# Optimization experiments

Hardware: AMD Instinct MI355X
Metric: run time of the kernel (lower is better)

The kernel has to match this reference:

```python
import jax, jax.numpy as jnp
import numpy as np

KS = 64      # kernel_size
NFFT = 64    # n_fft
IC = 32      # in_channel
OC = 64      # out_channel
B, T1, T2 = 4, 4096, 512


def setup_inputs() -> dict:
    key = jax.random.key(0)
    k1, k2, k3, k4 = jax.random.split(key, 4)
    x = jax.random.normal(k1, (B, T1, IC), dtype=jnp.float32)
    # continuous index in [0, T1-1)
    index = jax.random.uniform(k2, (B, T2), dtype=jnp.float32) * (T1 - 1)
    kb = 1.0 / np.sqrt(KS * IC)  # matches reset_parameters uniform bound
    kernel = jax.random.uniform(k3, (OC, IC, NFFT), minval=-kb, maxval=kb, dtype=jnp.float32)
    bias = jax.random.uniform(k4, (OC,), minval=-kb, maxval=kb, dtype=jnp.float32)
    return {"x": x, "index": index, "kernel": kernel, "bias": bias}


def reference(x, index, kernel, bias):
    # fractional-delay kernel per (b, t2) via FFT phase shift
    i = jnp.floor(index).astype(jnp.int32)          # (b, t2) integer part
    f = index - jnp.floor(index)                    # (b, t2) fractional part
    freqs = jnp.arange(NFFT // 2 + 1)               # rfft bins
    shift = jnp.exp(2j * jnp.pi * f[..., None] * freqs / NFFT)   # (b, t2, nf)
    K = jnp.fft.rfft(kernel)                        # (oc, ic, nf)
    K = K[None, None] * shift[:, :, None, None, :]  # (b, t2, oc, ic, nf)
    ker = jnp.fft.irfft(K, n=KS)                    # (b, t2, oc, ic, ks)

    # gather centered length-ks windows of x at integer positions i
    pad = KS // 2
    x_pad = jnp.pad(x, ((0, 0), (pad, pad), (0, 0)))            # (b, t1+2p, ic)
    pos = i[:, :, None] + jnp.arange(KS)[None, None, :]          # (b, t2, ks)
    barr = jnp.arange(x.shape[0])[:, None, None]
    xwin = x_pad[barr, pos]                                      # (b, t2, ks, ic)

    # per-position matmul: out[b,t,o] = sum_{c,k} ker[b,t,o,c,k] * xwin[b,t,k,c]
    out = jnp.einsum('btock,btkc->bto', ker, xwin) + bias
    return out
```

## Files before the change

### kernel.cpp

```cpp
#include <hip/hip_runtime.h>
#include <hip/hip_bf16.h>
#include <math.h>

#define B_   4
#define T1_  4096
#define T2_  512
#define IC_  32
#define OC_  64
#define KS_  64

typedef unsigned short u16;
typedef unsigned int   u32;
typedef __attribute__((ext_vector_type(8))) short  short8;
typedef __attribute__((ext_vector_type(4))) float  float4v;

__device__ __forceinline__ u16 f2bf(float f) {
    union { u32 u; float f; } v; v.f = f;
    u32 u = v.u;
    return (u16)((u + 0x7FFFu + ((u >> 16) & 1u)) >> 16);
}

#define PI_F 3.14159265358979323846f

__global__ __launch_bounds__(256) void prep_interp_kernel(
        const float* __restrict__ x, const float* __restrict__ index,
        const float* __restrict__ kern, u16* __restrict__ Y,
        u16* __restrict__ Bsz)
{
    __shared__ __align__(16) float w2[4][76];

    const int tid = threadIdx.x;

    if (blockIdx.x < 64) {
        int gid = blockIdx.x * 256 + tid;
        int o   = gid & 63;
        int cs8 = gid >> 6;
        const float* p = kern + (size_t)o * 2048 + cs8 * 8;
        float4 a = *(const float4*)p;
        float4 b = *(const float4*)(p + 4);
        u16* q = Bsz + (size_t)cs8 * 512 + o * 8;
        *(ushort4*)(q)     = make_ushort4(f2bf(a.x), f2bf(a.y), f2bf(a.z), f2bf(a.w));
        *(ushort4*)(q + 4) = make_ushort4(f2bf(b.x), f2bf(b.y), f2bf(b.z), f2bf(b.w));
        return;
    }

    const int pb   = blockIdx.x - 64;
    const int wv   = tid >> 6;
    const int lane = tid & 63;
    const int bt   = pb * 4 + wv;
    const int b    = bt >> 9;

    const float fidx = index[bt];
    const float flo  = floorf(fidx);
    const int   i0   = (int)flo;
    const float f    = fidx - flo;

    {
        const int t = lane;
        float wj;
        if (f <= 0.0f) {
            wj = (t == 0) ? 1.0f : 0.0f;
        } else {
            float spf = sinf(PI_F * f);
            float a   = PI_F * ((float)t + f) * (1.0f / 64.0f);
            wj = ((t & 1) ? -spf : spf) * cosf(a) / (64.0f * sinf(a));
        }
        w2[wv][t] = wj;
        if (t < 8) w2[wv][64 + t] = wj;
    }

    const int nm = lane & 15;
    const int q  = lane >> 4;

    short8 Afr[4];
    #pragma unroll
    for (int d = 0; d < 4; ++d) {
        const int o0 = (16 * d + q * 8 - nm) & 63;
        const float* wp = &w2[wv][o0];
        union { u16 u[8]; short8 s; } cv;
        #pragma unroll
        for (int j = 0; j < 8; ++j) cv.u[j] = f2bf(wp[j]);
        Afr[d] = cv.s;
    }

    short8 Bfr[2][2];
    #pragma unroll
    for (int kb = 0; kb < 2; ++kb) {
        #pragma unroll
        for (int nt = 0; nt < 2; ++nt) {
            const int c = nt * 16 + nm;
            union { u16 u[8]; short8 s; } cv;
            #pragma unroll
            for (int j = 0; j < 8; ++j) {
                int pos = i0 - 32 + kb * 32 + q * 8 + j;
                int pc  = min(max(pos, 0), T1_ - 1);
                float v = x[(size_t)(b * T1_ + pc) * IC_ + c];
                v = ((unsigned)pos < (unsigned)T1_) ? v : 0.0f;
                cv.u[j] = f2bf(v);
            }
            Bfr[kb][nt] = cv.s;
        }
    }

    float4v acc[4][2];
    #pragma unroll
    for (int mt = 0; mt < 4; ++mt)
        #pragma unroll
        for (int nt = 0; nt < 2; ++nt)
            acc[mt][nt] = (float4v){0.f, 0.f, 0.f, 0.f};
    #pragma unroll
    for (int kb = 0; kb < 2; ++kb)
        #pragma unroll
        for (int mt = 0; mt < 4; ++mt) {
            const int d = (2 * kb - mt) & 3;
            #pragma unroll
            for (int nt = 0; nt < 2; ++nt)
                acc[mt][nt] = __builtin_amdgcn_mfma_f32_16x16x32_bf16(
                                  Afr[d], Bfr[kb][nt], acc[mt][nt], 0, 0, 0);
        }

    #pragma unroll
    for (int mt = 0; mt < 4; ++mt)
        #pragma unroll
        for (int nt = 0; nt < 2; ++nt) {
            const int c = nt * 16 + nm;
            const int s = mt * 16 + q * 4;
            u32 d0 = (u32)f2bf(acc[mt][nt][0]) | ((u32)f2bf(acc[mt][nt][1]) << 16);
            u32 d1 = (u32)f2bf(acc[mt][nt][2]) | ((u32)f2bf(acc[mt][nt][3]) << 16);
            *(uint2*)(Y + (size_t)bt * 2048 + c * 64 + s) = make_uint2(d0, d1);
        }
}

__global__ __launch_bounds__(512, 2) void gemm_kernel(const u16* __restrict__ Y,
                                                      const u16* __restrict__ Bsz,
                                                      const float* __restrict__ bias,
                                                      float* __restrict__ out)
{
    __shared__ float red[8][4][16][17];

    const int tid  = threadIdx.x;
    const int w    = tid >> 6;
    const int lane = tid & 63;
    const int nm   = lane & 15;
    const int q    = lane >> 4;
    const int g    = blockIdx.x;

    const int pbA = (g & 7) + 8 * (4 * (g >> 3) + (nm >> 2));
    const int btA = 4 * pbA + (nm & 3);

    const int kb0 = w * 8;
    const u16* aptr = Y   + (size_t)btA * 2048 + kb0 * 32 + q * 8;
    const u16* bptr = Bsz + (size_t)kb0 * 2048 + q * 512 + nm * 8;

    short8 a[8], b[8][4];
    #pragma unroll
    for (int i = 0; i < 8; ++i) {
        a[i] = *(const short8*)(aptr + i * 32);
        #pragma unroll
        for (int n = 0; n < 4; ++n)
            b[i][n] = *(const short8*)(bptr + (size_t)i * 2048 + n * 128);
    }

    float4v acc0 = {0,0,0,0}, acc1 = {0,0,0,0}, acc2 = {0,0,0,0}, acc3 = {0,0,0,0};
    #pragma unroll
    for (int i = 0; i < 8; ++i) {
        acc0 = __builtin_amdgcn_mfma_f32_16x16x32_bf16(a[i], b[i][0], acc0, 0, 0, 0);
        acc1 = __builtin_amdgcn_mfma_f32_16x16x32_bf16(a[i], b[i][1], acc1, 0, 0, 0);
        acc2 = __builtin_amdgcn_mfma_f32_16x16x32_bf16(a[i], b[i][2], acc2, 0, 0, 0);
        acc3 = __builtin_amdgcn_mfma_f32_16x16x32_bf16(a[i], b[i][3], acc3, 0, 0, 0);
    }

    #pragma unroll
    for (int r = 0; r < 4; ++r) {
        const int row = q * 4 + r;
        red[w][0][row][nm] = acc0[r];
        red[w][1][row][nm] = acc1[r];
        red[w][2][row][nm] = acc2[r];
        red[w][3][row][nm] = acc3[r];
    }
    __syncthreads();

    #pragma unroll
    for (int e = tid; e < 1024; e += 512) {
        const int row = e >> 6;
        const int o   = e & 63;
        float s = bias[o];
        #pragma unroll
        for (int ww = 0; ww < 8; ++ww)
            s += red[ww][o >> 4][row][o & 15];
        const int pbo = (g & 7) + 8 * (4 * (g >> 3) + (row >> 2));
        const int bto = 4 * pbo + (row & 3);
        out[(size_t)bto * 64 + o] = s;
    }
}

extern "C" void kernel_launch(void* const* d_in, const int* in_sizes, int n_in,
                              void* d_out, int out_size, void* d_ws, size_t ws_size,
                              hipStream_t stream)
{
    const float* x     = (const float*)d_in[0];
    const float* index = (const float*)d_in[1];
    const float* kern  = (const float*)d_in[2];
    const float* bias  = (const float*)d_in[3];
    float* out = (float*)d_out;

    u16* Y   = (u16*)d_ws;
    u16* Bsz = (u16*)((char*)d_ws + (size_t)8 * 1024 * 1024);

    prep_interp_kernel<<<dim3(64 + B_ * T2_ / 4), dim3(256), 0, stream>>>(x, index, kern, Y, Bsz);
    gemm_kernel<<<dim3(128), dim3(512), 0, stream>>>(Y, Bsz, bias, out);
}
```

Baseline: 71.79 us.

## Fuse interpolation and kernel GEMM into one kernel with LDS-staged intermediate

After: 76.05 us. +5.9%, slower.

```diff
diff --git a/kernel.cpp b/kernel.cpp
--- a/kernel.cpp
+++ b/kernel.cpp
@@ -14,40 +14,29 @@
 typedef __attribute__((ext_vector_type(8))) short  short8;
 typedef __attribute__((ext_vector_type(4))) float  float4v;
 
+#define PI_F 3.14159265358979323846f
+
 __device__ __forceinline__ u16 f2bf(float f) {
     union { u32 u; float f; } v; v.f = f;
     u32 u = v.u;
     return (u16)((u + 0x7FFFu + ((u >> 16) & 1u)) >> 16);
 }
 
-#define PI_F 3.14159265358979323846f
-
-__global__ __launch_bounds__(256) void prep_interp_kernel(
+__global__ __launch_bounds__(512, 2) void fused_kernel(
         const float* __restrict__ x, const float* __restrict__ index,
-        const float* __restrict__ kern, u16* __restrict__ Y,
-        u16* __restrict__ Bsz)
+        const float* __restrict__ kern, const float* __restrict__ bias,
+        float* __restrict__ out)
 {
-    __shared__ __align__(16) float w2[4][76];
-
-    const int tid = threadIdx.x;
-
-    if (blockIdx.x < 64) {
-        int gid = blockIdx.x * 256 + tid;
-        int o   = gid & 63;
-        int cs8 = gid >> 6;
-        const float* p = kern + (size_t)o * 2048 + cs8 * 8;
-        float4 a = *(const float4*)p;
-        float4 b = *(const float4*)(p + 4);
-        u16* q = Bsz + (size_t)cs8 * 512 + o * 8;
-        *(ushort4*)(q)     = make_ushort4(f2bf(a.x), f2bf(a.y), f2bf(a.z), f2bf(a.w));
-        *(ushort4*)(q + 4) = make_ushort4(f2bf(b.x), f2bf(b.y), f2bf(b.z), f2bf(b.w));
-        return;
-    }
-
-    const int pb   = blockIdx.x - 64;
-    const int wv   = tid >> 6;
+    __shared__ __align__(16) u32 Ylds[8192];
+    __shared__ float w2[8][76];
+    __shared__ float red[8][4][8][17];
+
+    const int tid  = threadIdx.x;
+    const int w    = tid >> 6;
     const int lane = tid & 63;
-    const int bt   = pb * 4 + wv;
+    const int nm   = lane & 15;
+    const int q    = lane >> 4;
+    const int bt   = blockIdx.x * 8 + w;
     const int b    = bt >> 9;
 
     const float fidx = index[bt];
@@ -65,18 +54,15 @@
             float a   = PI_F * ((float)t + f) * (1.0f / 64.0f);
             wj = ((t & 1) ? -spf : spf) * cosf(a) / (64.0f * sinf(a));
         }
-        w2[wv][t] = wj;
-        if (t < 8) w2[wv][64 + t] = wj;
-    }
-
-    const int nm = lane & 15;
-    const int q  = lane >> 4;
+        w2[w][t] = wj;
+        if (t < 8) w2[w][64 + t] = wj;
+    }
 
     short8 Afr[4];
     #pragma unroll
     for (int d = 0; d < 4; ++d) {
         const int o0 = (16 * d + q * 8 - nm) & 63;
-        const float* wp = &w2[wv][o0];
+        const float* wp = &w2[w][o0];
         union { u16 u[8]; short8 s; } cv;
         #pragma unroll
         for (int j = 0; j < 8; ++j) cv.u[j] = f2bf(wp[j]);
@@ -85,7 +71,7 @@
 
     short8 Bfr[2][2];
     #pragma unroll
-    for (int kb = 0; kb < 2; ++kb) {
+    for (int kb = 0; kb < 2; ++kb)
         #pragma unroll
         for (int nt = 0; nt < 2; ++nt) {
             const int c = nt * 16 + nm;
@@ -100,7 +86,6 @@
             }
             Bfr[kb][nt] = cv.s;
         }
-    }
 
     float4v acc[4][2];
     #pragma unroll
@@ -123,75 +108,81 @@
     for (int mt = 0; mt < 4; ++mt)
         #pragma unroll
         for (int nt = 0; nt < 2; ++nt) {
-            const int c = nt * 16 + nm;
-            const int s = mt * 16 + q * 4;
-            u32 d0 = (u32)f2bf(acc[mt][nt][0]) | ((u32)f2bf(acc[mt][nt][1]) << 16);
-            u32 d1 = (u32)f2bf(acc[mt][nt][2]) | ((u32)f2bf(acc[mt][nt][3]) << 16);
-            *(uint2*)(Y + (size_t)bt * 2048 + c * 64 + s) = make_uint2(d0, d1);
-        }
-}
-
-__global__ __launch_bounds__(512, 2) void gemm_kernel(const u16* __restrict__ Y,
-                                                      const u16* __restrict__ Bsz,
-                                                      const float* __restrict__ bias,
-                                                      float* __restrict__ out)
-{
-    __shared__ float red[8][4][16][17];
-
-    const int tid  = threadIdx.x;
-    const int w    = tid >> 6;
-    const int lane = tid & 63;
-    const int nm   = lane & 15;
-    const int q    = lane >> 4;
-    const int g    = blockIdx.x;
-
-    const int pbA = (g & 7) + 8 * (4 * (g >> 3) + (nm >> 2));
-    const int btA = 4 * pbA + (nm & 3);
-
-    const int kb0 = w * 8;
-    const u16* aptr = Y   + (size_t)btA * 2048 + kb0 * 32 + q * 8;
-    const u16* bptr = Bsz + (size_t)kb0 * 2048 + q * 512 + nm * 8;
-
-    short8 a[8], b[8][4];
+            const int c   = nt * 16 + nm;
+            const int cs0 = c * 64 + mt * 16 + q * 4;
+            const u32 wi  = (u32)((cs0 >> 3) * 32 + ((w ^ (c & 7)) << 2) + ((q & 1) << 1));
+            const u32 d0  = (u32)f2bf(acc[mt][nt][0]) | ((u32)f2bf(acc[mt][nt][1]) << 16);
+            const u32 d1  = (u32)f2bf(acc[mt][nt][2]) | ((u32)f2bf(acc[mt][nt][3]) << 16);
+            *(uint2*)&Ylds[wi] = make_uint2(d0, d1);
+        }
+
+    const float4* bp = (const float4*)(kern + (size_t)nm * 2048 + w * 256 + q * 8);
+
+    float4 Bb[2][4][2];
+    #pragma unroll
+    for (int nt = 0; nt < 4; ++nt) {
+        Bb[0][nt][0] = bp[nt * 8192];
+        Bb[0][nt][1] = bp[nt * 8192 + 1];
+    }
+
+    __syncthreads();
+
+    const int rA = nm & 7;
+    short8 Aa[2];
+    {
+        const int kb = w * 8;
+        const u32 ab = (u32)(kb * 512 + q * 128 + ((rA ^ ((kb >> 1) & 7)) << 4));
+        Aa[0] = *(const short8*)((const char*)Ylds + ab);
+    }
+
+    float4v a2[4];
+    #pragma unroll
+    for (int nt = 0; nt < 4; ++nt) a2[nt] = (float4v){0.f, 0.f, 0.f, 0.f};
+
     #pragma unroll
     for (int i = 0; i < 8; ++i) {
-        a[i] = *(const short8*)(aptr + i * 32);
-        #pragma unroll
-        for (int n = 0; n < 4; ++n)
-            b[i][n] = *(const short8*)(bptr + (size_t)i * 2048 + n * 128);
-    }
-
-    float4v acc0 = {0,0,0,0}, acc1 = {0,0,0,0}, acc2 = {0,0,0,0}, acc3 = {0,0,0,0};
-    #pragma unroll
-    for (int i = 0; i < 8; ++i) {
-        acc0 = __builtin_amdgcn_mfma_f32_16x16x32_bf16(a[i], b[i][0], acc0, 0, 0, 0);
-        acc1 = __builtin_amdgcn_mfma_f32_16x16x32_bf16(a[i], b[i][1], acc1, 0, 0, 0);
-        acc2 = __builtin_amdgcn_mfma_f32_16x16x32_bf16(a[i], b[i][2], acc2, 0, 0, 0);
-        acc3 = __builtin_amdgcn_mfma_f32_16x16x32_bf16(a[i], b[i][3], acc3, 0, 0, 0);
-    }
-
-    #pragma unroll
-    for (int r = 0; r < 4; ++r) {
-        const int row = q * 4 + r;
-        red[w][0][row][nm] = acc0[r];
-        red[w][1][row][nm] = acc1[r];
-        red[w][2][row][nm] = acc2[r];
-        red[w][3][row][nm] = acc3[r];
+        const int cur = i & 1, nxt = cur ^ 1;
+        if (i < 7) {
+            const int i1 = i + 1;
+            const int fo = i1 * 8;
+            #pragma unroll
+            for (int nt = 0; nt < 4; ++nt) {
+                Bb[nxt][nt][0] = bp[nt * 8192 + fo];
+                Bb[nxt][nt][1] = bp[nt * 8192 + fo + 1];
+            }
+            const int kb = w * 8 + i1;
+            const u32 ab = (u32)(kb * 512 + q * 128 + ((rA ^ ((kb >> 1) & 7)) << 4));
+            Aa[nxt] = *(const short8*)((const char*)Ylds + ab);
+        }
+        #pragma unroll
+        for (int nt = 0; nt < 4; ++nt) {
+            union { u16 u[8]; short8 s; } cv;
+            cv.u[0] = f2bf(Bb[cur][nt][0].x);
+            cv.u[1] = f2bf(Bb[cur][nt][0].y);
+            cv.u[2] = f2bf(Bb[cur][nt][0].z);
+            cv.u[3] = f2bf(Bb[cur][nt][0].w);
+            cv.u[4] = f2bf(Bb[cur][nt][1].x);
+            cv.u[5] = f2bf(Bb[cur][nt][1].y);
+            cv.u[6] = f2bf(Bb[cur][nt][1].z);
+            cv.u[7] = f2bf(Bb[cur][nt][1].w);
+            a2[nt] = __builtin_amdgcn_mfma_f32_16x16x32_bf16(Aa[cur], cv.s, a2[nt], 0, 0, 0);
+        }
+    }
+
+    if (q < 2) {
+        #pragma unroll
+        for (int nt = 0; nt < 4; ++nt)
+            #pragma unroll
+            for (int r = 0; r < 4; ++r)
+                red[w][nt][q * 4 + r][nm] = a2[nt][r];
     }
     __syncthreads();
 
-    #pragma unroll
-    for (int e = tid; e < 1024; e += 512) {
-        const int row = e >> 6;
-        const int o   = e & 63;
-        float s = bias[o];
-        #pragma unroll
-        for (int ww = 0; ww < 8; ++ww)
-            s += red[ww][o >> 4][row][o & 15];
-        const int pbo = (g & 7) + 8 * (4 * (g >> 3) + (row >> 2));
-        const int bto = 4 * pbo + (row & 3);
-        out[(size_t)bto * 64 + o] = s;
-    }
+    float s = bias[lane];
+    #pragma unroll
+    for (int ww = 0; ww < 8; ++ww)
+        s += red[ww][q][w][nm];
+    out[(size_t)bt * 64 + lane] = s;
 }
 
 extern "C" void kernel_launch(void* const* d_in, const int* in_sizes, int n_in,
@@ -203,10 +194,7 @@
     const float* kern  = (const float*)d_in[2];
     const float* bias  = (const float*)d_in[3];
     float* out = (float*)d_out;
-
-    u16* Y   = (u16*)d_ws;
-    u16* Bsz = (u16*)((char*)d_ws + (size_t)8 * 1024 * 1024);
-
-    prep_interp_kernel<<<dim3(64 + B_ * T2_ / 4), dim3(256), 0, stream>>>(x, index, kern, Y, Bsz);
-    gemm_kernel<<<dim3(128), dim3(512), 0, stream>>>(Y, Bsz, bias, out);
+    (void)in_sizes; (void)n_in; (void)out_size; (void)d_ws; (void)ws_size;
+
+    fused_kernel<<<dim3(B_ * T2_ / 8), dim3(512), 0, stream>>>(x, index, kern, bias, out);
 }
```
